# Kernel tuning notes

Measured on AMD Instinct MI355X. Metric: run time of the kernel, lower is better.

## Reference

```python
import jax, jax.numpy as jnp
import numpy as np

EMBED_DIM = 1024
NUM_HEADS = 16
HEAD_DIM = EMBED_DIM // NUM_HEADS
BZ, Q_LEN, CACHE_LEN = 4, 512, 1536


def setup_inputs() -> dict:
    key = jax.random.key(0)
    ks = jax.random.split(key, 8)
    inp = {
        "hidden_states": jax.random.normal(ks[0], (BZ, Q_LEN, EMBED_DIM), jnp.float32),
        "attention_mask": jnp.zeros((BZ, 1, 1, CACHE_LEN + Q_LEN), jnp.float32),
        "k_cache": jax.random.normal(ks[1], (BZ, CACHE_LEN, EMBED_DIM), jnp.float32),
        "v_cache": jax.random.normal(ks[2], (BZ, CACHE_LEN, EMBED_DIM), jnp.float32),
        "Wq": jax.random.normal(ks[3], (EMBED_DIM, EMBED_DIM), jnp.float32) * 0.02,
        "bq": jnp.zeros((EMBED_DIM,), jnp.float32),
        "Wk": jax.random.normal(ks[4], (EMBED_DIM, EMBED_DIM), jnp.float32) * 0.02,
        "bk": jnp.zeros((EMBED_DIM,), jnp.float32),
        "Wv": jax.random.normal(ks[5], (EMBED_DIM, EMBED_DIM), jnp.float32) * 0.02,
        "bv": jnp.zeros((EMBED_DIM,), jnp.float32),
        "Wo": jax.random.normal(ks[6], (EMBED_DIM, EMBED_DIM), jnp.float32) * 0.02,
        "bo": jnp.zeros((EMBED_DIM,), jnp.float32),
    }
    return inp


def reference(hidden_states, attention_mask, k_cache, v_cache,
              Wq, bq, Wk, bk, Wv, bv, Wo, bo):
    bz, q_len, embed_dim = hidden_states.shape
    # projections (nn.Linear: x @ W.T + b)
    q = hidden_states @ Wq.T + bq
    k_new = hidden_states @ Wk.T + bk
    v_new = hidden_states @ Wv.T + bv
    # KV-cache concat (self_attn path)
    k = jnp.concatenate([k_cache, k_new], axis=1)  # [bz, kv_len, E]
    v = jnp.concatenate([v_cache, v_new], axis=1)
    q_begin = k_cache.shape[1]
    kv_len = k.shape[1]
    # split heads -> [bz, H, L, D]
    qh = q.reshape(bz, q_len, NUM_HEADS, HEAD_DIM).transpose(0, 2, 1, 3)
    kh = k.reshape(bz, kv_len, NUM_HEADS, HEAD_DIM).transpose(0, 2, 1, 3)
    vh = v.reshape(bz, kv_len, NUM_HEADS, HEAD_DIM).transpose(0, 2, 1, 3)
    scores = jnp.einsum("bhqd,bhkd->bhqk", qh, kh) / (HEAD_DIM ** 0.5)
    # causal mask slice causal_mask[q_begin:q_begin+q_len, :kv_len]
    rows = q_begin + jnp.arange(q_len)          # absolute query positions
    cols = jnp.arange(kv_len)
    causal = jnp.where(cols[None, :] > rows[:, None], -jnp.inf, 0.0).astype(scores.dtype)
    scores = scores + attention_mask + causal
    probs = jax.nn.softmax(scores, axis=-1)
    ctx = jnp.einsum("bhqk,bhkd->bhqd", probs, vh)
    ctx = ctx.transpose(0, 2, 1, 3).reshape(bz, q_len, embed_dim)
    out = ctx @ Wo.T + bo
    return out, k, v
```

## Files before the change

kernel.cpp:

```cpp
#include <hip/hip_runtime.h>
#include <hip/hip_bf16.h>
#include <stdint.h>

#define BZv 4
#define QL 512
#define CL 1536
#define KVL 2048
#define EMB 1024
#define NH 16
#define HD 64
#define QSCALE 0.18033688011112042f

typedef __attribute__((ext_vector_type(8))) short short8;
typedef __attribute__((ext_vector_type(4))) float floatx4;

__device__ __forceinline__ unsigned short f2b(float f) {
  union { float f; unsigned int u; } v; v.f = f;
  return (unsigned short)((v.u + 0x7FFFu + ((v.u >> 16) & 1u)) >> 16);
}

__device__ __forceinline__ ushort2 pk2(float a, float b) {
  union { __hip_bfloat162 h; ushort2 u; } c;
  c.h = __float22bfloat162_rn(make_float2(a, b));
  return c.u;
}

#if __has_builtin(__builtin_amdgcn_exp2f)
#define EXP2F(x) __builtin_amdgcn_exp2f(x)
#else
#define EXP2F(x) exp2f(x)
#endif

__device__ __forceinline__ void gload_lds16(const void* g, void* l) {
  __builtin_amdgcn_global_load_lds(
      (const __attribute__((address_space(1))) unsigned char*)g,
      (__attribute__((address_space(3))) unsigned char*)l, 16, 0, 0);
}

__global__ __launch_bounds__(256) void prep_kernel(
    const float* __restrict__ hid, const float* __restrict__ Wq, const float* __restrict__ Wk,
    const float* __restrict__ Wv, const float* __restrict__ Wo,
    const float* __restrict__ kc, const float* __restrict__ vc, const float* __restrict__ msk,
    unsigned short* __restrict__ Xb, unsigned short* __restrict__ Wqb, unsigned short* __restrict__ Wkb,
    unsigned short* __restrict__ Wvb, unsigned short* __restrict__ Wob,
    unsigned short* __restrict__ Kb, unsigned short* __restrict__ Vb,
    float* __restrict__ kf, float* __restrict__ vf, unsigned short* __restrict__ wb)
{
  const long HID4 = (long)BZv * QL * EMB / 4;
  const long W4   = (long)EMB * EMB / 4;
  const long C4   = (long)BZv * CL * EMB / 4;
  const long t0 = HID4, t1 = t0 + W4, t2 = t1 + W4, t3 = t2 + W4, t4 = t3 + W4;
  const long t5 = t4 + C4, t6 = t5 + C4;
  const long total = t6 + (long)BZv * KVL / 4;
  for (long i = (long)blockIdx.x * blockDim.x + threadIdx.x; i < total;
       i += (long)gridDim.x * blockDim.x) {
    if (i < t4) {
      const float* src; unsigned short* dst; long j;
      if (i < t0)      { src = hid; dst = Xb;  j = i; }
      else if (i < t1) { src = Wq;  dst = Wqb; j = i - t0; }
      else if (i < t2) { src = Wk;  dst = Wkb; j = i - t1; }
      else if (i < t3) { src = Wv;  dst = Wvb; j = i - t2; }
      else             { src = Wo;  dst = Wob; j = i - t3; }
      float4 v = ((const float4*)src)[j];
      ushort4 o; o.x = f2b(v.x); o.y = f2b(v.y); o.z = f2b(v.z); o.w = f2b(v.w);
      ((ushort4*)dst)[j] = o;
    } else if (i < t6) {
      bool isV = (i >= t5);
      long j = i - (isV ? t5 : t4);
      const float* src = isV ? vc : kc;
      float4 v = ((const float4*)src)[j];
      long e4 = j * 4;
      int b = (int)(e4 / ((long)CL * EMB));
      long rem = e4 - (long)b * CL * EMB;
      long doff = (long)b * KVL * EMB + rem;
      if (isV) {
        *((float4*)(vf + doff)) = v;
        int row = (int)(rem >> 10);
        float w = __expf(msk[b * KVL + row]);
        ushort4 o; o.x = f2b(v.x * w); o.y = f2b(v.y * w);
        o.z = f2b(v.z * w); o.w = f2b(v.w * w);
        *((ushort4*)(Vb + doff)) = o;
      } else {
        *((float4*)(kf + doff)) = v;
        ushort4 o; o.x = f2b(v.x); o.y = f2b(v.y); o.z = f2b(v.z); o.w = f2b(v.w);
        *((ushort4*)(Kb + doff)) = o;
      }
    } else {
      long j = i - t6;
      float4 m4 = ((const float4*)msk)[j];
      ushort4 o;
      o.x = f2b(__expf(m4.x)); o.y = f2b(__expf(m4.y));
      o.z = f2b(__expf(m4.z)); o.w = f2b(__expf(m4.w));
      ((ushort4*)wb)[j] = o;
    }
  }
}

__global__ __launch_bounds__(256) void qkv_gemm(
    const unsigned short* __restrict__ Xb,
    const unsigned short* __restrict__ Wqb, const unsigned short* __restrict__ Wkb,
    const unsigned short* __restrict__ Wvb,
    const float* __restrict__ bq, const float* __restrict__ bk, const float* __restrict__ bv,
    const float* __restrict__ msk,
    unsigned short* __restrict__ Qb, unsigned short* __restrict__ Kb, unsigned short* __restrict__ Vb,
    float* __restrict__ kf, float* __restrict__ vf)
{
  __shared__ unsigned short At[128 * 32];
  __shared__ unsigned short Bt[64 * 32];
  const int tid = threadIdx.x, lane = tid & 63, wave = tid >> 6;
  const int quad = lane >> 4, l = lane & 15;
  const int mat = blockIdx.x >> 4;
  const int ncol = (blockIdx.x & 15) * 64;
  const int mbase = blockIdx.y * 128;
  const unsigned short* W = (mat == 0) ? Wqb : (mat == 1) ? Wkb : Wvb;
  const float* bias = (mat == 0) ? bq : (mat == 1) ? bk : bv;
  const int srow = tid >> 2, slds = tid & 3;
  const int rh = wave * 32;

  floatx4 zero = {0.f, 0.f, 0.f, 0.f};
  floatx4 acc[2][4];
#pragma unroll
  for (int i = 0; i < 2; i++)
#pragma unroll
    for (int j = 0; j < 4; j++) acc[i][j] = zero;

  for (int k0 = 0; k0 < EMB; k0 += 32) {
    __syncthreads();
#pragma unroll
    for (int s = 0; s < 2; s++) {
      int row = s * 64 + srow;
      int gc = slds ^ (row & 3);
      gload_lds16(Xb + (size_t)(mbase + row) * EMB + k0 + gc * 8, &At[row * 32 + slds * 8]);
    }
    {
      int row = srow;
      int gc = slds ^ (row & 3);
      gload_lds16(W + (size_t)(ncol + row) * EMB + k0 + gc * 8, &Bt[row * 32 + slds * 8]);
    }
    __syncthreads();
    short8 af[2], bfr[4];
#pragma unroll
    for (int rt = 0; rt < 2; rt++) {
      int row = rh + rt * 16 + l;
      af[rt] = *(const short8*)&At[row * 32 + ((quad ^ (row & 3)) * 8)];
    }
#pragma unroll
    for (int ct = 0; ct < 4; ct++) {
      int row = ct * 16 + l;
      bfr[ct] = *(const short8*)&Bt[row * 32 + ((quad ^ (row & 3)) * 8)];
    }
#pragma unroll
    for (int rt = 0; rt < 2; rt++)
#pragma unroll
      for (int ct = 0; ct < 4; ct++)
        acc[rt][ct] = __builtin_amdgcn_mfma_f32_16x16x32_bf16(af[rt], bfr[ct], acc[rt][ct], 0, 0, 0);
  }

#pragma unroll
  for (int ct = 0; ct < 4; ct++) {
    int col = ncol + ct * 16 + l;
    float bb = bias[col];
#pragma unroll
    for (int rt = 0; rt < 2; rt++)
#pragma unroll
      for (int r = 0; r < 4; r++) {
        int m = mbase + rh + rt * 16 + quad * 4 + r;
        float val = acc[rt][ct][r] + bb;
        if (mat == 0) {
          Qb[(size_t)m * EMB + col] = f2b(val * QSCALE);
        } else {
          size_t a = ((size_t)(m >> 9) * KVL + CL + (m & 511)) * EMB + col;
          if (mat == 1) { Kb[a] = f2b(val); kf[a] = val; }
          else {
            float w = __expf(msk[(m >> 9) * KVL + CL + (m & 511)]);
            Vb[a] = f2b(val * w); vf[a] = val;
          }
        }
      }
  }
}

__global__ __launch_bounds__(256) void oproj_gemm(
    const unsigned short* __restrict__ A, const unsigned short* __restrict__ W,
    const float* __restrict__ bias, float* __restrict__ out)
{
  __shared__ unsigned short At[64 * 32];
  __shared__ unsigned short Bt[64 * 32];
  const int tid = threadIdx.x, lane = tid & 63, wave = tid >> 6;
  const int quad = lane >> 4, l = lane & 15;
  const int ncol = blockIdx.x * 64;
  const int mbase = blockIdx.y * 64;
  const int srow = tid >> 2, slds = tid & 3;
  const int rh = (wave & 1) * 32, ch = (wave >> 1) * 32;

  floatx4 zero = {0.f, 0.f, 0.f, 0.f};
  floatx4 acc[2][2];
#pragma unroll
  for (int i = 0; i < 2; i++)
#pragma unroll
    for (int j = 0; j < 2; j++) acc[i][j] = zero;

  for (int k0 = 0; k0 < EMB; k0 += 32) {
    __syncthreads();
    {
      int gc = slds ^ (srow & 3);
      gload_lds16(A + (size_t)(mbase + srow) * EMB + k0 + gc * 8, &At[srow * 32 + slds * 8]);
      gload_lds16(W + (size_t)(ncol + srow) * EMB + k0 + gc * 8, &Bt[srow * 32 + slds * 8]);
    }
    __syncthreads();
    short8 af[2], bfr[2];
#pragma unroll
    for (int rt = 0; rt < 2; rt++) {
      int row = rh + rt * 16 + l;
      af[rt] = *(const short8*)&At[row * 32 + ((quad ^ (row & 3)) * 8)];
    }
#pragma unroll
    for (int ct = 0; ct < 2; ct++) {
      int row = ch + ct * 16 + l;
      bfr[ct] = *(const short8*)&Bt[row * 32 + ((quad ^ (row & 3)) * 8)];
    }
#pragma unroll
    for (int rt = 0; rt < 2; rt++)
#pragma unroll
      for (int ct = 0; ct < 2; ct++)
        acc[rt][ct] = __builtin_amdgcn_mfma_f32_16x16x32_bf16(af[rt], bfr[ct], acc[rt][ct], 0, 0, 0);
  }

#pragma unroll
  for (int ct = 0; ct < 2; ct++) {
    int col = ncol + ch + ct * 16 + l;
    float bb = bias[col];
#pragma unroll
    for (int rt = 0; rt < 2; rt++)
#pragma unroll
      for (int r = 0; r < 4; r++) {
        int m = mbase + rh + rt * 16 + quad * 4 + r;
        out[(size_t)m * EMB + col] = acc[rt][ct][r] + bb;
      }
  }
}

__global__ __launch_bounds__(256) void attn_kernel(
    const unsigned short* __restrict__ Qb, const unsigned short* __restrict__ Kb,
    const unsigned short* __restrict__ Vb, const unsigned short* __restrict__ wb,
    unsigned short* __restrict__ Cb)
{
  __shared__ unsigned short Vt[2][66 * 72];
  __shared__ unsigned short Pl[4][16 * 72];
  const int id = blockIdx.x;
  const int hb = id & 63, qt = id >> 6;
  const int b = hb >> 4, h = hb & 15;
  const int tid = threadIdx.x, lane = tid & 63, wave = tid >> 6;
  const int quad = lane >> 4, l = lane & 15;
  const int qbase = qt * 64 + wave * 16;

  const unsigned short* qp = Qb + (size_t)(b * QL + qbase + l) * EMB + h * HD + quad * 8;
  const short8 bq0 = *(const short8*)qp;
  const short8 bq1 = *(const short8*)(qp + 32);

  floatx4 zero = {0.f, 0.f, 0.f, 0.f};
  floatx4 o[4], o4 = zero;
#pragma unroll
  for (int c = 0; c < 4; c++) o[c] = zero;
  float mr = -INFINITY;

  const int kv_end = CL + qt * 64 + 64;
  const int vp = tid & 31, vg = tid >> 5;
  const unsigned short* vsrc = Vb + (size_t)(b * KVL) * EMB + h * HD + vg * 8;
  const unsigned short* wsrc = wb + (size_t)b * KVL + 2 * vp;
  const unsigned short* kbase = Kb + (size_t)(b * KVL) * EMB + h * HD + quad * 8;

  uint4 va = *(const uint4*)(vsrc + (size_t)(2 * vp) * EMB);
  uint4 vbr = *(const uint4*)(vsrc + (size_t)(2 * vp + 1) * EMB);
  short8 kc[8];
#pragma unroll
  for (int c = 0; c < 4; c++) {
    const unsigned short* kp = kbase + (size_t)(c * 16 + l) * EMB;
    kc[2 * c] = *(const short8*)kp;
    kc[2 * c + 1] = *(const short8*)(kp + 32);
  }
  {
    const unsigned short* pa = (const unsigned short*)&va;
    const unsigned short* pb = (const unsigned short*)&vbr;
#pragma unroll
    for (int j = 0; j < 8; j++) {
      ushort2 t; t.x = pa[j]; t.y = pb[j];
      *(ushort2*)&Vt[0][(vg * 8 + j) * 72 + 2 * vp] = t;
    }
    if (vg == 0) *(ushort2*)&Vt[0][64 * 72 + 2 * vp] = *(const ushort2*)wsrc;
  }
  __syncthreads();

  int cur = 0;
  for (int kv0 = 0; kv0 < kv_end; kv0 += 64) {
    const bool more = (kv0 + 64 < kv_end);
    uint4 vna, vnb; ushort2 wn; short8 kn[8];
    if (more) {
      const unsigned short* vs = vsrc + (size_t)(kv0 + 64 + 2 * vp) * EMB;
      vna = *(const uint4*)vs;
      vnb = *(const uint4*)(vs + EMB);
      if (vg == 0) wn = *(const ushort2*)(wsrc + kv0 + 64);
#pragma unroll
      for (int c = 0; c < 4; c++) {
        const unsigned short* kp = kbase + (size_t)(kv0 + 64 + c * 16 + l) * EMB;
        kn[2 * c] = *(const short8*)kp;
        kn[2 * c + 1] = *(const short8*)(kp + 32);
      }
    }
    floatx4 s[4];
#pragma unroll
    for (int c = 0; c < 4; c++) {
      s[c] = __builtin_amdgcn_mfma_f32_16x16x32_bf16(kc[2 * c], bq0, zero, 0, 0, 0);
      s[c] = __builtin_amdgcn_mfma_f32_16x16x32_bf16(kc[2 * c + 1], bq1, s[c], 0, 0, 0);
    }
    if (kv0 + 63 > CL + qbase) {
      const int lim = CL + qbase + l;
#pragma unroll
      for (int c = 0; c < 4; c++) {
        int kvb = kv0 + c * 16 + quad * 4;
#pragma unroll
        for (int r = 0; r < 4; r++)
          s[c][r] = (kvb + r <= lim) ? s[c][r] : -INFINITY;
      }
    }
    float t0 = fmaxf(fmaxf(s[0][0], s[0][1]), fmaxf(s[0][2], s[0][3]));
    float t1 = fmaxf(fmaxf(s[1][0], s[1][1]), fmaxf(s[1][2], s[1][3]));
    float t2 = fmaxf(fmaxf(s[2][0], s[2][1]), fmaxf(s[2][2], s[2][3]));
    float t3 = fmaxf(fmaxf(s[3][0], s[3][1]), fmaxf(s[3][2], s[3][3]));
    float lmax = fmaxf(fmaxf(t0, t1), fmaxf(t2, t3));
    lmax = fmaxf(lmax, __shfl_xor(lmax, 16, 64));
    lmax = fmaxf(lmax, __shfl_xor(lmax, 32, 64));
    float mnew = fmaxf(mr, lmax);
    float alpha = EXP2F(mr - mnew);
    mr = mnew;
#pragma unroll
    for (int c = 0; c < 4; c++) {
      float p0 = EXP2F(s[c][0] - mnew), p1 = EXP2F(s[c][1] - mnew);
      float p2 = EXP2F(s[c][2] - mnew), p3 = EXP2F(s[c][3] - mnew);
      ushort2 lo = pk2(p0, p1), hi = pk2(p2, p3);
      ushort4 pk; pk.x = lo.x; pk.y = lo.y; pk.z = hi.x; pk.w = hi.y;
      *(ushort4*)&Pl[wave][l * 72 + c * 16 + quad * 4] = pk;
    }
#pragma unroll
    for (int c = 0; c < 4; c++)
#pragma unroll
      for (int r = 0; r < 4; r++) o[c][r] *= alpha;
#pragma unroll
    for (int r = 0; r < 4; r++) o4[r] *= alpha;
    asm volatile("s_waitcnt lgkmcnt(0)" ::: "memory");
    short8 pf0 = *(const short8*)&Pl[wave][l * 72 + quad * 8];
    short8 pf1 = *(const short8*)&Pl[wave][l * 72 + 32 + quad * 8];
    short8 vw0 = *(const short8*)&Vt[cur][64 * 72 + quad * 8];
    short8 vw1 = *(const short8*)&Vt[cur][64 * 72 + 32 + quad * 8];
    o4 = __builtin_amdgcn_mfma_f32_16x16x32_bf16(vw0, pf0, o4, 0, 0, 0);
    o4 = __builtin_amdgcn_mfma_f32_16x16x32_bf16(vw1, pf1, o4, 0, 0, 0);
#pragma unroll
    for (int c = 0; c < 4; c++) {
      short8 a0v = *(const short8*)&Vt[cur][(c * 16 + l) * 72 + quad * 8];
      short8 a1v = *(const short8*)&Vt[cur][(c * 16 + l) * 72 + 32 + quad * 8];
      o[c] = __builtin_amdgcn_mfma_f32_16x16x32_bf16(a0v, pf0, o[c], 0, 0, 0);
      o[c] = __builtin_amdgcn_mfma_f32_16x16x32_bf16(a1v, pf1, o[c], 0, 0, 0);
    }
    if (more) {
      const unsigned short* pa = (const unsigned short*)&vna;
      const unsigned short* pb = (const unsigned short*)&vnb;
#pragma unroll
      for (int j = 0; j < 8; j++) {
        ushort2 t; t.x = pa[j]; t.y = pb[j];
        *(ushort2*)&Vt[cur ^ 1][(vg * 8 + j) * 72 + 2 * vp] = t;
      }
      if (vg == 0) *(ushort2*)&Vt[cur ^ 1][64 * 72 + 2 * vp] = wn;
#pragma unroll
      for (int i = 0; i < 8; i++) kc[i] = kn[i];
    }
    __syncthreads();
    cur ^= 1;
  }

  float inv = 1.0f / o4[0];
  size_t qrow = (size_t)(b * QL + qbase + l) * EMB + h * HD;
#pragma unroll
  for (int c = 0; c < 4; c++)
#pragma unroll
    for (int r = 0; r < 4; r++)
      Cb[qrow + c * 16 + quad * 4 + r] = f2b(o[c][r] * inv);
}

extern "C" void kernel_launch(void* const* d_in, const int* in_sizes, int n_in,
                              void* d_out, int out_size, void* d_ws, size_t ws_size,
                              hipStream_t stream) {
  const float* hid  = (const float*)d_in[0];
  const float* mask = (const float*)d_in[1];
  const float* kc   = (const float*)d_in[2];
  const float* vc   = (const float*)d_in[3];
  const float* Wq   = (const float*)d_in[4];
  const float* bq   = (const float*)d_in[5];
  const float* Wk   = (const float*)d_in[6];
  const float* bk   = (const float*)d_in[7];
  const float* Wv   = (const float*)d_in[8];
  const float* bv   = (const float*)d_in[9];
  const float* Wo   = (const float*)d_in[10];
  const float* bo   = (const float*)d_in[11];

  float* out_f = (float*)d_out;
  float* kf = out_f + (size_t)BZv * QL * EMB;
  float* vf = kf + (size_t)BZv * KVL * EMB;

  char* p = (char*)d_ws;
  unsigned short* Xb  = (unsigned short*)p; p += (size_t)BZv * QL * EMB * 2;
  unsigned short* Wqb = (unsigned short*)p; p += (size_t)EMB * EMB * 2;
  unsigned short* Wkb = (unsigned short*)p; p += (size_t)EMB * EMB * 2;
  unsigned short* Wvb = (unsigned short*)p; p += (size_t)EMB * EMB * 2;
  unsigned short* Wob = (unsigned short*)p; p += (size_t)EMB * EMB * 2;
  unsigned short* Qb  = (unsigned short*)p; p += (size_t)BZv * QL * EMB * 2;
  unsigned short* Kb  = (unsigned short*)p; p += (size_t)BZv * KVL * EMB * 2;
  unsigned short* Vb  = (unsigned short*)p; p += (size_t)BZv * KVL * EMB * 2;
  unsigned short* Cb  = (unsigned short*)p; p += (size_t)BZv * QL * EMB * 2;
  unsigned short* wbp = (unsigned short*)p; p += (size_t)BZv * KVL * 2;

  prep_kernel<<<2048, 256, 0, stream>>>(hid, Wq, Wk, Wv, Wo, kc, vc, mask,
                                        Xb, Wqb, Wkb, Wvb, Wob, Kb, Vb, kf, vf, wbp);
  qkv_gemm<<<dim3(48, 16), 256, 0, stream>>>(Xb, Wqb, Wkb, Wvb, bq, bk, bv, mask,
                                             Qb, Kb, Vb, kf, vf);
  attn_kernel<<<512, 256, 0, stream>>>(Qb, Kb, Vb, wbp, Cb);
  oproj_gemm<<<dim3(16, 32), 256, 0, stream>>>(Cb, Wob, bo, out_f);
}
```

Baseline: 287.6 us.

## Split attention KV range into two segments with combine kernel and LDS K staging

Splits each attention block's KV loop into two halves (split-K / flash-decoding style), doubling the grid to 1024 blocks. Each half writes unnormalized partial outputs, running maxima and denominators to workspace, and a new combine kernel merges them into the bf16 context. K tiles are now loaded asynchronously into swizzled LDS via gload_lds16 instead of into registers, and V becomes single-buffered with an extra barrier per iteration. The aim is better occupancy and load balance across CUs. The cost is extra fp32 partial-result traffic and one more kernel launch.

Result: faster. 248.7 us (-13.5%).

```diff
diff --git a/kernel.cpp b/kernel.cpp
--- a/kernel.cpp
+++ b/kernel.cpp
@@ -10,6 +10,7 @@
 #define NH 16
 #define HD 64
 #define QSCALE 0.18033688011112042f
+#define NG 2048
 
 typedef __attribute__((ext_vector_type(8))) short short8;
 typedef __attribute__((ext_vector_type(4))) float floatx4;
@@ -240,20 +241,29 @@
   }
 }
 
-__global__ __launch_bounds__(256) void attn_kernel(
+__global__ __launch_bounds__(256, 4) void attn_kernel(
     const unsigned short* __restrict__ Qb, const unsigned short* __restrict__ Kb,
     const unsigned short* __restrict__ Vb, const unsigned short* __restrict__ wb,
-    unsigned short* __restrict__ Cb)
+    float* __restrict__ PO, float* __restrict__ PM, float* __restrict__ PD)
 {
-  __shared__ unsigned short Vt[2][66 * 72];
+  __shared__ unsigned short Kt[2][64 * 64];
+  __shared__ unsigned short Vt[65 * 72];
   __shared__ unsigned short Pl[4][16 * 72];
-  const int id = blockIdx.x;
+
+  const int bid = blockIdx.x;
+  const int seg = bid >> 9;
+  const int id = bid & 511;
   const int hb = id & 63, qt = id >> 6;
   const int b = hb >> 4, h = hb & 15;
   const int tid = threadIdx.x, lane = tid & 63, wave = tid >> 6;
   const int quad = lane >> 4, l = lane & 15;
   const int qbase = qt * 64 + wave * 16;
 
+  const int nt_tot = (CL >> 6) + qt + 1;
+  const int n0 = nt_tot >> 1;
+  const int t_beg = seg ? n0 : 0;
+  const int t_end = seg ? nt_tot : n0;
+
   const unsigned short* qp = Qb + (size_t)(b * QL + qbase + l) * EMB + h * HD + quad * 8;
   const short8 bq0 = *(const short8*)qp;
   const short8 bq1 = *(const short8*)(qp + 32);
@@ -264,54 +274,60 @@
   for (int c = 0; c < 4; c++) o[c] = zero;
   float mr = -INFINITY;
 
-  const int kv_end = CL + qt * 64 + 64;
   const int vp = tid & 31, vg = tid >> 5;
   const unsigned short* vsrc = Vb + (size_t)(b * KVL) * EMB + h * HD + vg * 8;
   const unsigned short* wsrc = wb + (size_t)b * KVL + 2 * vp;
-  const unsigned short* kbase = Kb + (size_t)(b * KVL) * EMB + h * HD + quad * 8;
-
-  uint4 va = *(const uint4*)(vsrc + (size_t)(2 * vp) * EMB);
-  uint4 vbr = *(const uint4*)(vsrc + (size_t)(2 * vp + 1) * EMB);
-  short8 kc[8];
-#pragma unroll
-  for (int c = 0; c < 4; c++) {
-    const unsigned short* kp = kbase + (size_t)(c * 16 + l) * EMB;
-    kc[2 * c] = *(const short8*)kp;
-    kc[2 * c + 1] = *(const short8*)(kp + 32);
-  }
-  {
+  const unsigned short* ksrc = Kb + (size_t)(b * KVL) * EMB + h * HD;
+  const int sw = l & 7;
+
+  uint4 va, vbr; ushort2 wn;
+  auto VLOAD = [&](int t) {
+    const unsigned short* vs = vsrc + (size_t)(t * 64 + 2 * vp) * EMB;
+    va = *(const uint4*)vs;
+    vbr = *(const uint4*)(vs + EMB);
+    if (vg == 0) wn = *(const ushort2*)(wsrc + t * 64);
+  };
+  auto VSTAGE = [&]() {
     const unsigned short* pa = (const unsigned short*)&va;
     const unsigned short* pb = (const unsigned short*)&vbr;
 #pragma unroll
     for (int j = 0; j < 8; j++) {
-      ushort2 t; t.x = pa[j]; t.y = pb[j];
-      *(ushort2*)&Vt[0][(vg * 8 + j) * 72 + 2 * vp] = t;
-    }
-    if (vg == 0) *(ushort2*)&Vt[0][64 * 72 + 2 * vp] = *(const ushort2*)wsrc;
-  }
+      ushort2 tt; tt.x = pa[j]; tt.y = pb[j];
+      *(ushort2*)&Vt[(vg * 8 + j) * 72 + 2 * vp] = tt;
+    }
+    if (vg == 0) *(ushort2*)&Vt[64 * 72 + 2 * vp] = wn;
+  };
+  auto GLOAD_K = [&](int t, int buf) {
+    const int kv0 = t * 64;
+#pragma unroll
+    for (int s = 0; s < 2; s++) {
+      int g = s * 256 + tid;
+      int r = g >> 3, k = g & 7;
+      gload_lds16(ksrc + (size_t)(kv0 + r) * EMB + ((k ^ (r & 7)) * 8),
+                  &Kt[buf][g * 8]);
+    }
+  };
+
+  VLOAD(t_beg);
+  GLOAD_K(t_beg, 0);
   __syncthreads();
+  VSTAGE();
+  if (t_beg + 1 < t_end) VLOAD(t_beg + 1);
+  __syncthreads();
 
   int cur = 0;
-  for (int kv0 = 0; kv0 < kv_end; kv0 += 64) {
-    const bool more = (kv0 + 64 < kv_end);
-    uint4 vna, vnb; ushort2 wn; short8 kn[8];
-    if (more) {
-      const unsigned short* vs = vsrc + (size_t)(kv0 + 64 + 2 * vp) * EMB;
-      vna = *(const uint4*)vs;
-      vnb = *(const uint4*)(vs + EMB);
-      if (vg == 0) wn = *(const ushort2*)(wsrc + kv0 + 64);
-#pragma unroll
-      for (int c = 0; c < 4; c++) {
-        const unsigned short* kp = kbase + (size_t)(kv0 + 64 + c * 16 + l) * EMB;
-        kn[2 * c] = *(const short8*)kp;
-        kn[2 * c + 1] = *(const short8*)(kp + 32);
-      }
-    }
+  for (int t = t_beg; t < t_end; ++t) {
+    if (t + 1 < t_end) GLOAD_K(t + 1, cur ^ 1);
+    const int kv0 = t * 64;
     floatx4 s[4];
 #pragma unroll
     for (int c = 0; c < 4; c++) {
-      s[c] = __builtin_amdgcn_mfma_f32_16x16x32_bf16(kc[2 * c], bq0, zero, 0, 0, 0);
-      s[c] = __builtin_amdgcn_mfma_f32_16x16x32_bf16(kc[2 * c + 1], bq1, s[c], 0, 0, 0);
+      const int rr = c * 16 + l;
+      const unsigned short* krow = &Kt[cur][rr * 64];
+      short8 k0 = *(const short8*)&krow[(quad ^ sw) * 8];
+      short8 k1 = *(const short8*)&krow[((quad + 4) ^ sw) * 8];
+      s[c] = __builtin_amdgcn_mfma_f32_16x16x32_bf16(k0, bq0, zero, 0, 0, 0);
+      s[c] = __builtin_amdgcn_mfma_f32_16x16x32_bf16(k1, bq1, s[c], 0, 0, 0);
     }
     if (kv0 + 63 > CL + qbase) {
       const int lim = CL + qbase + l;
@@ -323,11 +339,11 @@
           s[c][r] = (kvb + r <= lim) ? s[c][r] : -INFINITY;
       }
     }
-    float t0 = fmaxf(fmaxf(s[0][0], s[0][1]), fmaxf(s[0][2], s[0][3]));
-    float t1 = fmaxf(fmaxf(s[1][0], s[1][1]), fmaxf(s[1][2], s[1][3]));
-    float t2 = fmaxf(fmaxf(s[2][0], s[2][1]), fmaxf(s[2][2], s[2][3]));
-    float t3 = fmaxf(fmaxf(s[3][0], s[3][1]), fmaxf(s[3][2], s[3][3]));
-    float lmax = fmaxf(fmaxf(t0, t1), fmaxf(t2, t3));
+    float u0 = fmaxf(fmaxf(s[0][0], s[0][1]), fmaxf(s[0][2], s[0][3]));
+    float u1 = fmaxf(fmaxf(s[1][0], s[1][1]), fmaxf(s[1][2], s[1][3]));
+    float u2 = fmaxf(fmaxf(s[2][0], s[2][1]), fmaxf(s[2][2], s[2][3]));
+    float u3 = fmaxf(fmaxf(s[3][0], s[3][1]), fmaxf(s[3][2], s[3][3]));
+    float lmax = fmaxf(fmaxf(u0, u1), fmaxf(u2, u3));
     lmax = fmaxf(lmax, __shfl_xor(lmax, 16, 64));
     lmax = fmaxf(lmax, __shfl_xor(lmax, 32, 64));
     float mnew = fmaxf(mr, lmax);
@@ -350,40 +366,71 @@
     asm volatile("s_waitcnt lgkmcnt(0)" ::: "memory");
     short8 pf0 = *(const short8*)&Pl[wave][l * 72 + quad * 8];
     short8 pf1 = *(const short8*)&Pl[wave][l * 72 + 32 + quad * 8];
-    short8 vw0 = *(const short8*)&Vt[cur][64 * 72 + quad * 8];
-    short8 vw1 = *(const short8*)&Vt[cur][64 * 72 + 32 + quad * 8];
+    short8 vw0 = *(const short8*)&Vt[64 * 72 + quad * 8];
+    short8 vw1 = *(const short8*)&Vt[64 * 72 + 32 + quad * 8];
     o4 = __builtin_amdgcn_mfma_f32_16x16x32_bf16(vw0, pf0, o4, 0, 0, 0);
     o4 = __builtin_amdgcn_mfma_f32_16x16x32_bf16(vw1, pf1, o4, 0, 0, 0);
 #pragma unroll
     for (int c = 0; c < 4; c++) {
-      short8 a0v = *(const short8*)&Vt[cur][(c * 16 + l) * 72 + quad * 8];
-      short8 a1v = *(const short8*)&Vt[cur][(c * 16 + l) * 72 + 32 + quad * 8];
+      short8 a0v = *(const short8*)&Vt[(c * 16 + l) * 72 + quad * 8];
+      short8 a1v = *(const short8*)&Vt[(c * 16 + l) * 72 + 32 + quad * 8];
       o[c] = __builtin_amdgcn_mfma_f32_16x16x32_bf16(a0v, pf0, o[c], 0, 0, 0);
       o[c] = __builtin_amdgcn_mfma_f32_16x16x32_bf16(a1v, pf1, o[c], 0, 0, 0);
     }
-    if (more) {
-      const unsigned short* pa = (const unsigned short*)&vna;
-      const unsigned short* pb = (const unsigned short*)&vnb;
-#pragma unroll
-      for (int j = 0; j < 8; j++) {
-        ushort2 t; t.x = pa[j]; t.y = pb[j];
-        *(ushort2*)&Vt[cur ^ 1][(vg * 8 + j) * 72 + 2 * vp] = t;
-      }
-      if (vg == 0) *(ushort2*)&Vt[cur ^ 1][64 * 72 + 2 * vp] = wn;
-#pragma unroll
-      for (int i = 0; i < 8; i++) kc[i] = kn[i];
+    __syncthreads();
+    if (t + 1 < t_end) {
+      VSTAGE();
+      if (t + 2 < t_end) VLOAD(t + 2);
     }
     __syncthreads();
     cur ^= 1;
   }
 
-  float inv = 1.0f / o4[0];
-  size_t qrow = (size_t)(b * QL + qbase + l) * EMB + h * HD;
+  const int gid = hb * 32 + qt * 4 + wave;
+  float* po = PO + ((size_t)(seg * NG + gid)) * 1024 + l * 64;
 #pragma unroll
   for (int c = 0; c < 4; c++)
-#pragma unroll
-    for (int r = 0; r < 4; r++)
-      Cb[qrow + c * 16 + quad * 4 + r] = f2b(o[c][r] * inv);
+    *(floatx4*)&po[c * 16 + quad * 4] = o[c];
+  if (quad == 0) {
+    PM[(size_t)(seg * NG + gid) * 16 + l] = mr;
+    PD[(size_t)(seg * NG + gid) * 16 + l] = o4[0];
+  }
+}
+
+__global__ __launch_bounds__(256) void attn_combine(
+    const float* __restrict__ PO, const float* __restrict__ PM, const float* __restrict__ PD,
+    unsigned short* __restrict__ Cb)
+{
+  const int tid = threadIdx.x, wave = tid >> 6, lane = tid & 63;
+  const int quad = lane >> 4, l = lane & 15;
+  const int gid = blockIdx.x * 4 + wave;
+  const int hb = gid >> 5, qt = (gid >> 2) & 7, wv = gid & 3;
+  const int b = hb >> 4, h = hb & 15;
+  const int q = qt * 64 + wv * 16 + l;
+
+  float m0 = PM[(size_t)gid * 16 + l];
+  float m1 = PM[(size_t)(NG + gid) * 16 + l];
+  float d0 = PD[(size_t)gid * 16 + l];
+  float d1 = PD[(size_t)(NG + gid) * 16 + l];
+  float M = fmaxf(m0, m1);
+  float a0 = EXP2F(m0 - M), a1 = EXP2F(m1 - M);
+  float inv = 1.0f / (d0 * a0 + d1 * a1);
+  a0 *= inv; a1 *= inv;
+
+  const float* p0 = PO + (size_t)gid * 1024 + l * 64 + quad * 16;
+  const float* p1 = p0 + (size_t)NG * 1024;
+  unsigned short* cp = Cb + (size_t)(b * QL + q) * EMB + h * HD + quad * 16;
+#pragma unroll
+  for (int v = 0; v < 4; v++) {
+    float4 x0 = *(const float4*)(p0 + v * 4);
+    float4 x1 = *(const float4*)(p1 + v * 4);
+    ushort4 w4;
+    w4.x = f2b(x0.x * a0 + x1.x * a1);
+    w4.y = f2b(x0.y * a0 + x1.y * a1);
+    w4.z = f2b(x0.z * a0 + x1.z * a1);
+    w4.w = f2b(x0.w * a0 + x1.w * a1);
+    *(ushort4*)(cp + v * 4) = w4;
+  }
 }
 
 extern "C" void kernel_launch(void* const* d_in, const int* in_sizes, int n_in,
@@ -417,11 +464,15 @@
   unsigned short* Vb  = (unsigned short*)p; p += (size_t)BZv * KVL * EMB * 2;
   unsigned short* Cb  = (unsigned short*)p; p += (size_t)BZv * QL * EMB * 2;
   unsigned short* wbp = (unsigned short*)p; p += (size_t)BZv * KVL * 2;
+  float* POp = (float*)p; p += (size_t)2 * NG * 1024 * 4;
+  float* PMp = (float*)p; p += (size_t)2 * NG * 16 * 4;
+  float* PDp = (float*)p; p += (size_t)2 * NG * 16 * 4;
 
   prep_kernel<<<2048, 256, 0, stream>>>(hid, Wq, Wk, Wv, Wo, kc, vc, mask,
                                         Xb, Wqb, Wkb, Wvb, Wob, Kb, Vb, kf, vf, wbp);
   qkv_gemm<<<dim3(48, 16), 256, 0, stream>>>(Xb, Wqb, Wkb, Wvb, bq, bk, bv, mask,
                                              Qb, Kb, Vb, kf, vf);
-  attn_kernel<<<512, 256, 0, stream>>>(Qb, Kb, Vb, wbp, Cb);
+  attn_kernel<<<1024, 256, 0, stream>>>(Qb, Kb, Vb, wbp, POp, PMp, PDp);
+  attn_combine<<<512, 256, 0, stream>>>(POp, PMp, PDp, Cb);
   oproj_gemm<<<dim3(16, 32), 256, 0, stream>>>(Cb, Wob, bo, out_f);
 }
```
